# Optimization experiments

Hardware: AMD Instinct MI355X
Metric: run time of the kernel (lower is better)

## Reference

```python
import math
import jax, jax.numpy as jnp
import numpy as np

H = 8  # num_heads

def _layernorm(x, scale, bias, eps=1e-5):
    m = x.mean(-1, keepdims=True)
    v = x.var(-1, keepdims=True)
    return (x - m) / jnp.sqrt(v + eps) * scale + bias

def setup_inputs() -> dict:
    key = jax.random.key(0)
    ks = jax.random.split(key, 12)
    B, C, P, D, G = 8, 32, 256, 256, 512
    n = jax.random.normal
    return {
        "qz": n(ks[0], (B, C, P, D), dtype=jnp.float32),
        "unary": n(ks[1], (B, C, P, D), dtype=jnp.float32),
        # per-sample condition-instantiated factors; scaled ~1/sqrt(D) so attn logits are sane
        "time_u": n(ks[2], (B, D, D), dtype=jnp.float32) * 0.06,
        "time_v": n(ks[3], (B, D, D), dtype=jnp.float32) * 0.06,
        "channel_u": n(ks[4], (B, D, D), dtype=jnp.float32) * 0.06,
        "channel_v": n(ks[5], (B, D, D), dtype=jnp.float32) * 0.06,
        "topic_binary": n(ks[6], (B, G, D), dtype=jnp.float32) * 0.02,
        "norm_scale": jnp.ones((D,), jnp.float32),
        "norm_bias": jnp.zeros((D,), jnp.float32),
        "gate_w": n(ks[7], (D, D), dtype=jnp.float32) * 0.02,
        "gate_b": jnp.zeros((D,), jnp.float32),
        "out_w1": n(ks[8], (D, D), dtype=jnp.float32) * 0.02,
        "out_b1": jnp.zeros((D,), jnp.float32),
        "out_w2": n(ks[9], (D, D), dtype=jnp.float32) * 0.02,
        "out_b2": jnp.zeros((D,), jnp.float32),
    }

def reference(qz, unary, time_u, time_v, channel_u, channel_v, topic_binary,
              norm_scale, norm_bias, gate_w, gate_b, out_w1, out_b1, out_w2, out_b2):
    B, C, P, D = qz.shape
    R = D // H
    inv_sqrt_r = 1.0 / math.sqrt(R)

    qz_n = _layernorm(qz, norm_scale, norm_bias)

    def heads(x, w):  # [B,C,P,D] x [B,D,D] -> [B,C,P,H,R]
        return jnp.einsum('bcpd,bod->bcpo', x, w).reshape(B, C, P, H, R)

    # --- time-factor message: attention over P within each (b, c, h) ---
    qu = heads(qz_n, time_u).transpose(0, 1, 3, 2, 4)   # [B,C,H,P,R]
    qv = heads(qz_n, time_v).transpose(0, 1, 3, 2, 4)
    attn_t = jax.nn.softmax(jnp.einsum('bchpr,bchqr->bchpq', qu, qv) * inv_sqrt_r, axis=-1)
    m_t = jnp.einsum('bchpq,bcqd->bchpd', attn_t, qz_n).mean(axis=2)  # [B,C,P,D]

    # --- channel-factor message: attention over C within each (b, p, h) ---
    qu = heads(qz_n, channel_u).transpose(0, 2, 3, 1, 4)  # [B,P,H,C,R]
    qv = heads(qz_n, channel_v).transpose(0, 2, 3, 1, 4)
    attn_c = jax.nn.softmax(jnp.einsum('bphcr,bphfr->bphcf', qu, qv) * inv_sqrt_r, axis=-1)
    qzp = qz_n.transpose(0, 2, 1, 3)                      # [B,P,C,D]
    m_c = jnp.einsum('bphcf,bpfd->bphcd', attn_c, qzp).mean(axis=2).transpose(0, 2, 1, 3)

    # --- topic-modeling binary factor with AbsNormalize (relu + L1-normalize) ---
    qg = jax.nn.relu(jnp.einsum('bcpd,bgd->bcpg', qz_n, topic_binary))
    qg = qg / jnp.maximum(qg.sum(axis=-1, keepdims=True), 1e-6)
    m_g = jnp.einsum('bcpg,bgd->bcpd', qg, topic_binary)

    # --- gated residual update ---
    gate = jax.nn.sigmoid(qz @ gate_w.T + gate_b)
    qz2 = gate * qz + (1.0 - gate) * (unary + m_t + m_c + m_g)

    # --- output MLP with shared LayerNorm ---
    h = _layernorm(qz2, norm_scale, norm_bias)
    h = jax.nn.gelu(h @ out_w1.T + out_b1, approximate=False) @ out_w2.T + out_b2
    return qz2 + h
```

## Files before the change

kernel.cpp:

```cpp
#include <hip/hip_runtime.h>
#include <math.h>

namespace {

constexpr float INV_SQRT_R = 0.17677669529663689f;

typedef __attribute__((ext_vector_type(8))) __bf16 bf16x8;
typedef __attribute__((ext_vector_type(4))) float f32x4;

static __device__ __forceinline__ f32x4 MF(bf16x8 a, bf16x8 b, f32x4 c) {
    return __builtin_amdgcn_mfma_f32_16x16x32_bf16(a, b, c, 0, 0, 0);
}

__global__ __launch_bounds__(256) void cvt_kernel(
    const float* __restrict__ src, __bf16* __restrict__ dst, int n)
{
    int i = (blockIdx.x * 256 + threadIdx.x) * 4;
    if (i < n) {
        float4 v = *(const float4*)(src + i);
        dst[i + 0] = (__bf16)v.x; dst[i + 1] = (__bf16)v.y;
        dst[i + 2] = (__bf16)v.z; dst[i + 3] = (__bf16)v.w;
    }
}

__global__ __launch_bounds__(256) void cvt2_kernel(
    const float* __restrict__ src, __bf16* __restrict__ dst, int n,
    int dstChunk, int dstOff)
{
    int i = (blockIdx.x * 256 + threadIdx.x) * 4;
    if (i < n) {
        float4 v = *(const float4*)(src + i);
        int o = (i >> 16) * dstChunk + dstOff + (i & 65535);
        dst[o + 0] = (__bf16)v.x; dst[o + 1] = (__bf16)v.y;
        dst[o + 2] = (__bf16)v.z; dst[o + 3] = (__bf16)v.w;
    }
}

__global__ __launch_bounds__(256) void ln_kernel(
    const float* __restrict__ x, const float* __restrict__ sc,
    const float* __restrict__ bi, __bf16* __restrict__ y)
{
    const size_t row = blockIdx.x;
    const int t = threadIdx.x;
    const float v = x[row * 256 + t];
    float s = v, s2 = v * v;
    #pragma unroll
    for (int o = 32; o > 0; o >>= 1) {
        s  += __shfl_xor(s, o);
        s2 += __shfl_xor(s2, o);
    }
    __shared__ float ps[4], ps2[4];
    if ((t & 63) == 0) { ps[t >> 6] = s; ps2[t >> 6] = s2; }
    __syncthreads();
    const float S  = ps[0] + ps[1] + ps[2] + ps[3];
    const float S2 = ps2[0] + ps2[1] + ps2[2] + ps2[3];
    const float mean = S * (1.0f / 256.0f);
    const float var  = S2 * (1.0f / 256.0f) - mean * mean;
    const float inv  = 1.0f / sqrtf(var + 1e-5f);
    y[row * 256 + t] = (__bf16)((v - mean) * inv * sc[t] + bi[t]);
}

__global__ __launch_bounds__(256) void tpose_bf_kernel(
    const __bf16* __restrict__ src, __bf16* __restrict__ dst, int R, int C)
{
    const size_t bz = blockIdx.z;
    src += bz * (size_t)R * C;
    dst += bz * (size_t)R * C;
    __shared__ __bf16 tile[32][34];
    const int r0 = blockIdx.x * 32, c0 = blockIdx.y * 32;
    const int tx = threadIdx.x & 31, ty = threadIdx.x >> 5;
    #pragma unroll
    for (int i = 0; i < 32; i += 8)
        tile[ty + i][tx] = src[(size_t)(r0 + ty + i) * C + c0 + tx];
    __syncthreads();
    #pragma unroll
    for (int i = 0; i < 32; i += 8)
        dst[(size_t)(c0 + ty + i) * R + r0 + tx] = tile[tx][ty + i];
}

__global__ __launch_bounds__(256) void tpose_cvt_kernel(
    const float* __restrict__ src, __bf16* __restrict__ dst, int R, int C)
{
    const size_t bz = blockIdx.z;
    src += bz * (size_t)R * C;
    dst += bz * (size_t)R * C;
    __shared__ __bf16 tile[32][34];
    const int r0 = blockIdx.x * 32, c0 = blockIdx.y * 32;
    const int tx = threadIdx.x & 31, ty = threadIdx.x >> 5;
    #pragma unroll
    for (int i = 0; i < 32; i += 8)
        tile[ty + i][tx] = (__bf16)src[(size_t)(r0 + ty + i) * C + c0 + tx];
    __syncthreads();
    #pragma unroll
    for (int i = 0; i < 32; i += 8)
        dst[(size_t)(c0 + ty + i) * R + r0 + tx] = tile[tx][ty + i];
}

__global__ __launch_bounds__(256) void mgemm_kernel(
    const __bf16* __restrict__ A, const __bf16* __restrict__ Bm, __bf16* __restrict__ Cout,
    int K, size_t aStride, size_t bStride,
    size_t s_b, size_t s_c, size_t s_p, size_t s_w, size_t s_h)
{
    const int bb = blockIdx.z;
    const int m0 = blockIdx.x * 64;
    const int n0 = blockIdx.y * 256;
    const __bf16* Ab = A + (size_t)bb * aStride;
    const __bf16* Bb = Bm + (size_t)bb * bStride;
    __shared__ __align__(16) __bf16 As[64][40];
    __shared__ __align__(16) __bf16 Bs[256][40];
    const int t = threadIdx.x;
    const int lane = t & 63;
    const int wid = t >> 6;
    const int l15 = lane & 15, lg = lane >> 4;

    f32x4 acc[4][4] = {};

    for (int k0 = 0; k0 < K; k0 += 32) {
        {
            const int row = t >> 2, k8 = (t & 3) << 3;
            *(bf16x8*)&As[row][k8] = *(const bf16x8*)(Ab + (size_t)(m0 + row) * K + k0 + k8);
        }
        #pragma unroll
        for (int s = 0; s < 4; ++s) {
            const int slot = s * 256 + t;
            const int row = slot >> 2, k8 = (slot & 3) << 3;
            *(bf16x8*)&Bs[row][k8] = *(const bf16x8*)(Bb + (size_t)(n0 + row) * K + k0 + k8);
        }
        __syncthreads();
        bf16x8 af[4], bfr[4];
        #pragma unroll
        for (int i = 0; i < 4; ++i)
            af[i] = *(const bf16x8*)&As[i * 16 + l15][lg * 8];
        #pragma unroll
        for (int j = 0; j < 4; ++j)
            bfr[j] = *(const bf16x8*)&Bs[wid * 64 + j * 16 + l15][lg * 8];
        #pragma unroll
        for (int i = 0; i < 4; ++i)
            #pragma unroll
            for (int j = 0; j < 4; ++j)
                acc[i][j] = MF(af[i], bfr[j], acc[i][j]);
        __syncthreads();
    }

    #pragma unroll
    for (int j = 0; j < 4; ++j) {
        const int n = n0 + wid * 64 + j * 16 + l15;
        const size_t offn = (size_t)(n >> 8) * s_w + (size_t)((n >> 5) & 7) * s_h + (n & 31);
        #pragma unroll
        for (int i = 0; i < 4; ++i) {
            #pragma unroll
            for (int r = 0; r < 4; ++r) {
                const int m = m0 + i * 16 + lg * 4 + r;
                const size_t off = (size_t)bb * s_b + (size_t)(m >> 8) * s_c
                                 + (size_t)(m & 255) * s_p + offn;
                Cout[off] = (__bf16)acc[i][j][r];
            }
        }
    }
}

__global__ __launch_bounds__(256) void time_attn_mfma_kernel(
    const __bf16* __restrict__ qu, const __bf16* __restrict__ qv, __bf16* __restrict__ abar)
{
    const int bc = blockIdx.x;
    const int p0 = blockIdx.y * 64;
    const __bf16* quB = qu + (size_t)bc * 65536;
    const __bf16* qvB = qv + (size_t)bc * 65536;
    __shared__ __align__(16) __bf16 Us[64][40];
    __shared__ __align__(16) __bf16 Vs[256][40];
    const int t = threadIdx.x;
    const int lane = t & 63;
    const int wid = t >> 6;
    const int l15 = lane & 15, lg = lane >> 4;

    f32x4 acc[16] = {};

    for (int h = 0; h < 8; ++h) {
        const __bf16* quH = quB + h * 8192;
        const __bf16* qvH = qvB + h * 8192;
        __syncthreads();
        {
            const int row = t >> 2, k8 = (t & 3) << 3;
            *(bf16x8*)&Us[row][k8] = *(const bf16x8*)(quH + (size_t)(p0 + row) * 32 + k8);
        }
        #pragma unroll
        for (int i = 0; i < 4; ++i) {
            const int slot = i * 256 + t;
            const int row = slot >> 2, k8 = (slot & 3) << 3;
            *(bf16x8*)&Vs[row][k8] = *(const bf16x8*)(qvH + (size_t)row * 32 + k8);
        }
        __syncthreads();

        f32x4 s[16];
        bf16x8 a = *(const bf16x8*)&Us[wid * 16 + l15][lg * 8];
        #pragma unroll
        for (int j = 0; j < 16; ++j) {
            bf16x8 bfr = *(const bf16x8*)&Vs[j * 16 + l15][lg * 8];
            s[j] = MF(a, bfr, (f32x4){0.f, 0.f, 0.f, 0.f});
        }

        #pragma unroll
        for (int r = 0; r < 4; ++r) {
            float e[16];
            float sum = 0.0f;
            #pragma unroll
            for (int j = 0; j < 16; ++j) {
                e[j] = __expf(s[j][r] * INV_SQRT_R);
                sum += e[j];
            }
            sum += __shfl_xor(sum, 1);
            sum += __shfl_xor(sum, 2);
            sum += __shfl_xor(sum, 4);
            sum += __shfl_xor(sum, 8);
            const float inv = 0.125f / sum;
            #pragma unroll
            for (int j = 0; j < 16; ++j) acc[j][r] += e[j] * inv;
        }
    }

    __bf16* dst = abar + (size_t)bc * 65536 + (size_t)(p0 + wid * 16 + lg * 4) * 256 + l15;
    #pragma unroll
    for (int r = 0; r < 4; ++r)
        #pragma unroll
        for (int j = 0; j < 16; ++j)
            dst[(size_t)r * 256 + j * 16] = (__bf16)acc[j][r];
}

__global__ __launch_bounds__(256) void chan_fused_kernel(
    const __bf16* __restrict__ quc, const __bf16* __restrict__ qvc,
    const __bf16* __restrict__ qzn, __bf16* __restrict__ m_c)
{
    const int bp = blockIdx.x;
    const int b = bp >> 8, p = bp & 255;
    const __bf16* quB = quc + (size_t)bp * 8192;
    const __bf16* qvB = qvc + (size_t)bp * 8192;
    __shared__ float U[16896];
    __shared__ float ab[32 * 33];
    float* qus = U;
    float* qvs = U + 8448;
    const int t = threadIdx.x;
    #pragma unroll
    for (int i = 0; i < 4; ++i) {
        int fi = i * 256 + t;
        int e = fi << 3;
        bf16x8 a = *(const bf16x8*)(quB + e);
        bf16x8 bv = *(const bf16x8*)(qvB + e);
        int base = ((e >> 10) * 32 + ((e >> 5) & 31)) * 33 + (e & 31);
        #pragma unroll
        for (int j = 0; j < 8; ++j) {
            qus[base + j] = (float)a[j];
            qvs[base + j] = (float)bv[j];
        }
    }
    __syncthreads();
    const int c = t >> 3, j = t & 7;
    float acc[4] = {0.f, 0.f, 0.f, 0.f};
    for (int h = 0; h < 8; ++h) {
        float qur[32];
        #pragma unroll
        for (int r = 0; r < 32; ++r) qur[r] = qus[(h * 32 + c) * 33 + r];
        float s[4];
        #pragma unroll
        for (int jj = 0; jj < 4; ++jj) {
            int f = j * 4 + jj;
            const float* qvR = &qvs[(h * 32 + f) * 33];
            float a = 0.f;
            #pragma unroll
            for (int r = 0; r < 32; ++r) a += qur[r] * qvR[r];
            s[jj] = a * INV_SQRT_R;
        }
        float mx = fmaxf(fmaxf(s[0], s[1]), fmaxf(s[2], s[3]));
        mx = fmaxf(mx, __shfl_xor(mx, 1));
        mx = fmaxf(mx, __shfl_xor(mx, 2));
        mx = fmaxf(mx, __shfl_xor(mx, 4));
        float e0x = __expf(s[0] - mx), e1x = __expf(s[1] - mx);
        float e2x = __expf(s[2] - mx), e3x = __expf(s[3] - mx);
        float sum = e0x + e1x + e2x + e3x;
        sum += __shfl_xor(sum, 1);
        sum += __shfl_xor(sum, 2);
        sum += __shfl_xor(sum, 4);
        float inv = 0.125f / sum;
        acc[0] += e0x * inv; acc[1] += e1x * inv; acc[2] += e2x * inv; acc[3] += e3x * inv;
    }
    #pragma unroll
    for (int jj = 0; jj < 4; ++jj) ab[c * 33 + j * 4 + jj] = acc[jj];
    __syncthreads();
    float* bt = U;
    #pragma unroll 4
    for (int f = 0; f < 32; ++f)
        bt[f * 256 + t] = (float)qzn[((size_t)(b * 32 + f) * 256 + p) * 256 + t];
    __syncthreads();
    for (int c2 = 0; c2 < 32; c2 += 2) {
        float a0 = 0.f, a1 = 0.f;
        #pragma unroll
        for (int f = 0; f < 32; ++f) {
            float v = bt[f * 256 + t];
            a0 += ab[c2 * 33 + f] * v;
            a1 += ab[(c2 + 1) * 33 + f] * v;
        }
        size_t off = ((size_t)(b * 32 + c2) * 256 + p) * 256 + t;
        m_c[off] = (__bf16)a0;
        m_c[off + 65536] = (__bf16)a1;
    }
}

__global__ __launch_bounds__(256, 2) void topic_fused_kernel(
    const __bf16* __restrict__ qzn, const __bf16* __restrict__ topicb,
    const __bf16* __restrict__ topicTb, __bf16* __restrict__ m_g)
{
    const int bb = blockIdx.z;
    const int m0 = blockIdx.x * 32;
    const __bf16* Ab = qzn + (size_t)bb * 2097152;
    const __bf16* B1 = topicb + (size_t)bb * 131072;
    const __bf16* B2 = topicTb + (size_t)bb * 131072;
    __shared__ __align__(16) __bf16 As[32][40];
    __shared__ __align__(16) __bf16 Bs[512][40];
    __shared__ __align__(16) __bf16 Ps[32][520];
    __shared__ float rsInv[32];
    const int t = threadIdx.x;
    const int lane = t & 63, wid = t >> 6;
    const int l15 = lane & 15, lg = lane >> 4;

    f32x4 acc[2][8] = {};
    for (int k0 = 0; k0 < 256; k0 += 32) {
        if (t < 128) {
            const int row = t >> 2, k8 = (t & 3) << 3;
            *(bf16x8*)&As[row][k8] = *(const bf16x8*)(Ab + (size_t)(m0 + row) * 256 + k0 + k8);
        }
        #pragma unroll
        for (int s = 0; s < 8; ++s) {
            const int slot = s * 256 + t;
            const int row = slot >> 2, k8 = (slot & 3) << 3;
            *(bf16x8*)&Bs[row][k8] = *(const bf16x8*)(B1 + (size_t)row * 256 + k0 + k8);
        }
        __syncthreads();
        bf16x8 af0 = *(const bf16x8*)&As[l15][lg * 8];
        bf16x8 af1 = *(const bf16x8*)&As[16 + l15][lg * 8];
        #pragma unroll
        for (int j = 0; j < 8; ++j) {
            bf16x8 b8 = *(const bf16x8*)&Bs[wid * 128 + j * 16 + l15][lg * 8];
            acc[0][j] = MF(af0, b8, acc[0][j]);
            acc[1][j] = MF(af1, b8, acc[1][j]);
        }
        __syncthreads();
    }
    #pragma unroll
    for (int i = 0; i < 2; ++i)
        #pragma unroll
        for (int j = 0; j < 8; ++j) {
            const int n = wid * 128 + j * 16 + l15;
            #pragma unroll
            for (int r = 0; r < 4; ++r)
                Ps[i * 16 + lg * 4 + r][n] = (__bf16)fmaxf(acc[i][j][r], 0.0f);
        }
    __syncthreads();
    {
        const int row = t >> 3, seg = t & 7;
        float s = 0.0f;
        #pragma unroll
        for (int u = 0; u < 8; ++u) {
            bf16x8 v = *(const bf16x8*)&Ps[row][seg * 64 + u * 8];
            #pragma unroll
            for (int e = 0; e < 8; ++e) s += (float)v[e];
        }
        s += __shfl_xor(s, 1);
        s += __shfl_xor(s, 2);
        s += __shfl_xor(s, 4);
        if (seg == 0) rsInv[row] = 1.0f / fmaxf(s, 1e-6f);
    }
    __syncthreads();
    f32x4 acc2[2][4] = {};
    for (int k0 = 0; k0 < 512; k0 += 32) {
        #pragma unroll
        for (int s = 0; s < 4; ++s) {
            const int slot = s * 256 + t;
            const int row = slot >> 2, k8 = (slot & 3) << 3;
            *(bf16x8*)&Bs[row][k8] = *(const bf16x8*)(B2 + (size_t)row * 512 + k0 + k8);
        }
        __syncthreads();
        bf16x8 af0 = *(const bf16x8*)&Ps[l15][k0 + lg * 8];
        bf16x8 af1 = *(const bf16x8*)&Ps[16 + l15][k0 + lg * 8];
        #pragma unroll
        for (int j = 0; j < 4; ++j) {
            bf16x8 b8 = *(const bf16x8*)&Bs[wid * 64 + j * 16 + l15][lg * 8];
            acc2[0][j] = MF(af0, b8, acc2[0][j]);
            acc2[1][j] = MF(af1, b8, acc2[1][j]);
        }
        __syncthreads();
    }
    #pragma unroll
    for (int i = 0; i < 2; ++i)
        #pragma unroll
        for (int j = 0; j < 4; ++j) {
            const int n = wid * 64 + j * 16 + l15;
            #pragma unroll
            for (int r = 0; r < 4; ++r) {
                const int ml = i * 16 + lg * 4 + r;
                m_g[(size_t)bb * 2097152 + (size_t)(m0 + ml) * 256 + n]
                    = (__bf16)(acc2[i][j][r] * rsInv[ml]);
            }
        }
}

__global__ __launch_bounds__(256, 2) void mega_kernel(
    const __bf16* __restrict__ qzb, const float* __restrict__ unary,
    const __bf16* __restrict__ m_t, const __bf16* __restrict__ m_c,
    const __bf16* __restrict__ m_g,
    const __bf16* __restrict__ gwb, const float* __restrict__ gate_b,
    const __bf16* __restrict__ w1b, const float* __restrict__ b1,
    const __bf16* __restrict__ w2b, const float* __restrict__ b2,
    const float* __restrict__ nsc, const float* __restrict__ nbi,
    float* __restrict__ outp)
{
    const int m0 = blockIdx.x * 64;
    __shared__ __align__(16) __bf16 As[64][40];
    __shared__ __align__(16) __bf16 Bs[256][40];
    __shared__ __align__(16) __bf16 hL[64][264];
    __shared__ float lnp[64][4][2];
    const int t = threadIdx.x;
    const int lane = t & 63, wid = t >> 6;
    const int l15 = lane & 15, lg = lane >> 4;

    f32x4 acc[4][4] = {};
    for (int k0 = 0; k0 < 256; k0 += 32) {
        {
            const int row = t >> 2, k8 = (t & 3) << 3;
            *(bf16x8*)&As[row][k8] = *(const bf16x8*)(qzb + (size_t)(m0 + row) * 256 + k0 + k8);
        }
        #pragma unroll
        for (int s = 0; s < 4; ++s) {
            const int slot = s * 256 + t;
            const int row = slot >> 2, k8 = (slot & 3) << 3;
            *(bf16x8*)&Bs[row][k8] = *(const bf16x8*)(gwb + (size_t)row * 256 + k0 + k8);
        }
        __syncthreads();
        bf16x8 af[4], bfr[4];
        #pragma unroll
        for (int i = 0; i < 4; ++i) af[i] = *(const bf16x8*)&As[i * 16 + l15][lg * 8];
        #pragma unroll
        for (int j = 0; j < 4; ++j) bfr[j] = *(const bf16x8*)&Bs[wid * 64 + j * 16 + l15][lg * 8];
        #pragma unroll
        for (int i = 0; i < 4; ++i)
            #pragma unroll
            for (int j = 0; j < 4; ++j)
                acc[i][j] = MF(af[i], bfr[j], acc[i][j]);
        __syncthreads();
    }

    f32x4 z2[4][4];
    #pragma unroll
    for (int i = 0; i < 4; ++i) {
        #pragma unroll
        for (int r = 0; r < 4; ++r) {
            float s = 0.0f, s2 = 0.0f;
            #pragma unroll
            for (int j = 0; j < 4; ++j) {
                const int n = wid * 64 + j * 16 + l15;
                const size_t off = (size_t)(m0 + i * 16 + lg * 4 + r) * 256 + n;
                float g = 1.0f / (1.0f + __expf(-(acc[i][j][r] + gate_b[n])));
                float rest = unary[off] + (float)m_t[off] + (float)m_c[off] + (float)m_g[off];
                float v = g * (float)qzb[off] + (1.0f - g) * rest;
                z2[i][j][r] = v;
                s += v; s2 += v * v;
            }
            s  += __shfl_xor(s, 1);  s  += __shfl_xor(s, 2);
            s  += __shfl_xor(s, 4);  s  += __shfl_xor(s, 8);
            s2 += __shfl_xor(s2, 1); s2 += __shfl_xor(s2, 2);
            s2 += __shfl_xor(s2, 4); s2 += __shfl_xor(s2, 8);
            if (l15 == 0) {
                lnp[i * 16 + lg * 4 + r][wid][0] = s;
                lnp[i * 16 + lg * 4 + r][wid][1] = s2;
            }
        }
    }
    __syncthreads();
    #pragma unroll
    for (int i = 0; i < 4; ++i) {
        #pragma unroll
        for (int r = 0; r < 4; ++r) {
            const int rr = i * 16 + lg * 4 + r;
            float S  = lnp[rr][0][0] + lnp[rr][1][0] + lnp[rr][2][0] + lnp[rr][3][0];
            float S2 = lnp[rr][0][1] + lnp[rr][1][1] + lnp[rr][2][1] + lnp[rr][3][1];
            float mean = S * (1.0f / 256.0f);
            float var  = S2 * (1.0f / 256.0f) - mean * mean;
            float inv  = 1.0f / sqrtf(var + 1e-5f);
            #pragma unroll
            for (int j = 0; j < 4; ++j) {
                const int n = wid * 64 + j * 16 + l15;
                hL[rr][n] = (__bf16)((z2[i][j][r] - mean) * inv * nsc[n] + nbi[n]);
            }
        }
    }
    __syncthreads();

    f32x4 acc2[4][4] = {};
    for (int k0 = 0; k0 < 256; k0 += 32) {
        #pragma unroll
        for (int s = 0; s < 4; ++s) {
            const int slot = s * 256 + t;
            const int row = slot >> 2, k8 = (slot & 3) << 3;
            *(bf16x8*)&Bs[row][k8] = *(const bf16x8*)(w1b + (size_t)row * 256 + k0 + k8);
        }
        __syncthreads();
        bf16x8 af[4], bfr[4];
        #pragma unroll
        for (int i = 0; i < 4; ++i) af[i] = *(const bf16x8*)&hL[i * 16 + l15][k0 + lg * 8];
        #pragma unroll
        for (int j = 0; j < 4; ++j) bfr[j] = *(const bf16x8*)&Bs[wid * 64 + j * 16 + l15][lg * 8];
        #pragma unroll
        for (int i = 0; i < 4; ++i)
            #pragma unroll
            for (int j = 0; j < 4; ++j)
                acc2[i][j] = MF(af[i], bfr[j], acc2[i][j]);
        __syncthreads();
    }
    #pragma unroll
    for (int i = 0; i < 4; ++i)
        #pragma unroll
        for (int j = 0; j < 4; ++j) {
            const int n = wid * 64 + j * 16 + l15;
            const float bn = b1[n];
            #pragma unroll
            for (int r = 0; r < 4; ++r) {
                float x = acc2[i][j][r] + bn;
                hL[i * 16 + lg * 4 + r][n] = (__bf16)(0.5f * x * (1.0f + erff(x * 0.7071067811865475f)));
            }
        }
    __syncthreads();

    f32x4 acc3[4][4] = {};
    for (int k0 = 0; k0 < 256; k0 += 32) {
        #pragma unroll
        for (int s = 0; s < 4; ++s) {
            const int slot = s * 256 + t;
            const int row = slot >> 2, k8 = (slot & 3) << 3;
            *(bf16x8*)&Bs[row][k8] = *(const bf16x8*)(w2b + (size_t)row * 256 + k0 + k8);
        }
        __syncthreads();
        bf16x8 af[4], bfr[4];
        #pragma unroll
        for (int i = 0; i < 4; ++i) af[i] = *(const bf16x8*)&hL[i * 16 + l15][k0 + lg * 8];
        #pragma unroll
        for (int j = 0; j < 4; ++j) bfr[j] = *(const bf16x8*)&Bs[wid * 64 + j * 16 + l15][lg * 8];
        #pragma unroll
        for (int i = 0; i < 4; ++i)
            #pragma unroll
            for (int j = 0; j < 4; ++j)
                acc3[i][j] = MF(af[i], bfr[j], acc3[i][j]);
        __syncthreads();
    }
    #pragma unroll
    for (int i = 0; i < 4; ++i)
        #pragma unroll
        for (int j = 0; j < 4; ++j) {
            const int n = wid * 64 + j * 16 + l15;
            const float bn = b2[n];
            #pragma unroll
            for (int r = 0; r < 4; ++r) {
                const size_t off = (size_t)(m0 + i * 16 + lg * 4 + r) * 256 + n;
                outp[off] = z2[i][j][r] + acc3[i][j][r] + bn;
            }
        }
}

}

extern "C" void kernel_launch(void* const* d_in, const int* in_sizes, int n_in,
                              void* d_out, int out_size, void* d_ws, size_t ws_size,
                              hipStream_t stream)
{
    (void)in_sizes; (void)n_in; (void)out_size; (void)ws_size;
    const float* qz     = (const float*)d_in[0];
    const float* unary  = (const float*)d_in[1];
    const float* time_u = (const float*)d_in[2];
    const float* time_v = (const float*)d_in[3];
    const float* chan_u = (const float*)d_in[4];
    const float* chan_v = (const float*)d_in[5];
    const float* topic  = (const float*)d_in[6];
    const float* nsc    = (const float*)d_in[7];
    const float* nbi    = (const float*)d_in[8];
    const float* gate_w = (const float*)d_in[9];
    const float* gate_b = (const float*)d_in[10];
    const float* w1     = (const float*)d_in[11];
    const float* b1     = (const float*)d_in[12];
    const float* w2     = (const float*)d_in[13];
    const float* b2     = (const float*)d_in[14];

    char* base = (char*)d_ws;
    __bf16* qzn_b  = (__bf16*)base;
    __bf16* pool   = (__bf16*)(base + (32ull << 20));
    __bf16* wtime  = pool;
    __bf16* wchan  = pool + 1048576;
    __bf16* topicb = pool + 2097152;
    __bf16* topicTb= pool + 3145728;
    __bf16* gwb    = pool + 4194304;
    __bf16* w1b    = pool + 4259840;
    __bf16* w2b    = pool + 4325376;
    __bf16* Blo    = (__bf16*)(base + (64ull << 20));
    __bf16* Bhi    = (__bf16*)(base + (96ull << 20));
    __bf16* qu_t   = Blo;
    __bf16* qv_t   = Bhi;
    __bf16* qznT   = Blo;
    __bf16* qu_c   = Blo;
    __bf16* qv_c   = Bhi;
    __bf16* qzb    = Blo;
    __bf16* m_g    = Bhi;
    __bf16* m_t    = (__bf16*)(base + (128ull << 20));
    __bf16* m_c    = (__bf16*)(base + (160ull << 20));
    __bf16* abar   = (__bf16*)d_out;
    float*  OUTF   = (float*)d_out;

    dim3 blk(256);

    cvt2_kernel<<<512, blk, 0, stream>>>(time_u, wtime, 524288, 131072, 0);
    cvt2_kernel<<<512, blk, 0, stream>>>(time_v, wtime, 524288, 131072, 65536);
    cvt2_kernel<<<512, blk, 0, stream>>>(chan_u, wchan, 524288, 131072, 0);
    cvt2_kernel<<<512, blk, 0, stream>>>(chan_v, wchan, 524288, 131072, 65536);
    cvt_kernel<<<1024, blk, 0, stream>>>(topic, topicb, 1048576);
    tpose_cvt_kernel<<<dim3(16, 8, 8), blk, 0, stream>>>(topic, topicTb, 512, 256);
    cvt_kernel<<<64, blk, 0, stream>>>(gate_w, gwb, 65536);
    cvt_kernel<<<64, blk, 0, stream>>>(w1, w1b, 65536);
    cvt_kernel<<<64, blk, 0, stream>>>(w2, w2b, 65536);

    ln_kernel<<<65536, blk, 0, stream>>>(qz, nsc, nbi, qzn_b);

    mgemm_kernel<<<dim3(128, 2, 8), blk, 0, stream>>>(
        qzn_b, wtime, qu_t, 256, 2097152, 131072,
        2097152, 65536, 32, 16777216, 8192);

    time_attn_mfma_kernel<<<dim3(256, 4), blk, 0, stream>>>(qu_t, qv_t, abar);

    tpose_bf_kernel<<<dim3(8, 8, 256), blk, 0, stream>>>(qzn_b, qznT, 256, 256);

    mgemm_kernel<<<dim3(4, 1, 256), blk, 0, stream>>>(
        abar, qznT, m_t, 256, 65536, 65536,
        65536, 0, 256, 0, 32);

    mgemm_kernel<<<dim3(128, 2, 8), blk, 0, stream>>>(
        qzn_b, wchan, qu_c, 256, 2097152, 131072,
        2097152, 32, 8192, 16777216, 1024);

    chan_fused_kernel<<<2048, blk, 0, stream>>>(qu_c, qv_c, qzn_b, m_c);

    topic_fused_kernel<<<dim3(256, 1, 8), blk, 0, stream>>>(qzn_b, topicb, topicTb, m_g);

    cvt_kernel<<<16384, blk, 0, stream>>>(qz, qzb, 16777216);

    mega_kernel<<<1024, blk, 0, stream>>>(
        qzb, unary, m_t, m_c, m_g,
        gwb, gate_b, w1b, b1, w2b, b2, nsc, nbi, OUTF);
}
```

Measured before the change: 589.3 us.

## Fuse time-attention with m_t GEMM and fold qz conversion into mega kernel

The time-attention kernel now keeps its head-averaged attention matrix in shared memory and multiplies it directly by the transposed normalized input, removing the intermediate abar write/read and a separate GEMM launch. The mega kernel reads fp32 qz and converts it to bf16 in shared memory, eliminating a standalone conversion pass. The channel kernel stores q tiles as bf16 with vector loads instead of scalar fp32 expansion. Workspace buffers are re-aliased to fit the new schedule, and the larger shared memory footprint may reduce occupancy.

```diff
diff --git a/kernel.cpp b/kernel.cpp
--- a/kernel.cpp
+++ b/kernel.cpp
@@ -159,15 +159,20 @@
     }
 }
 
-__global__ __launch_bounds__(256) void time_attn_mfma_kernel(
-    const __bf16* __restrict__ qu, const __bf16* __restrict__ qv, __bf16* __restrict__ abar)
+__global__ __launch_bounds__(256) void time_attn_mt_kernel(
+    const __bf16* __restrict__ qu, const __bf16* __restrict__ qv,
+    const __bf16* __restrict__ qznT, __bf16* __restrict__ m_t)
 {
     const int bc = blockIdx.x;
     const int p0 = blockIdx.y * 64;
     const __bf16* quB = qu + (size_t)bc * 65536;
     const __bf16* qvB = qv + (size_t)bc * 65536;
-    __shared__ __align__(16) __bf16 Us[64][40];
-    __shared__ __align__(16) __bf16 Vs[256][40];
+    const __bf16* BT  = qznT + (size_t)bc * 65536;
+    __shared__ __align__(16) __bf16 R1[27136];
+    __bf16* Us  = R1;
+    __bf16* Vs  = R1 + 2560;
+    __bf16* aL  = R1;
+    __bf16* Bs2 = R1 + 16896;
     const int t = threadIdx.x;
     const int lane = t & 63;
     const int wid = t >> 6;
@@ -181,21 +186,21 @@
         __syncthreads();
         {
             const int row = t >> 2, k8 = (t & 3) << 3;
-            *(bf16x8*)&Us[row][k8] = *(const bf16x8*)(quH + (size_t)(p0 + row) * 32 + k8);
+            *(bf16x8*)&Us[row * 40 + k8] = *(const bf16x8*)(quH + (size_t)(p0 + row) * 32 + k8);
         }
         #pragma unroll
         for (int i = 0; i < 4; ++i) {
             const int slot = i * 256 + t;
             const int row = slot >> 2, k8 = (slot & 3) << 3;
-            *(bf16x8*)&Vs[row][k8] = *(const bf16x8*)(qvH + (size_t)row * 32 + k8);
+            *(bf16x8*)&Vs[row * 40 + k8] = *(const bf16x8*)(qvH + (size_t)row * 32 + k8);
         }
         __syncthreads();
 
         f32x4 s[16];
-        bf16x8 a = *(const bf16x8*)&Us[wid * 16 + l15][lg * 8];
+        bf16x8 a = *(const bf16x8*)&Us[(wid * 16 + l15) * 40 + lg * 8];
         #pragma unroll
         for (int j = 0; j < 16; ++j) {
-            bf16x8 bfr = *(const bf16x8*)&Vs[j * 16 + l15][lg * 8];
+            bf16x8 bfr = *(const bf16x8*)&Vs[(j * 16 + l15) * 40 + lg * 8];
             s[j] = MF(a, bfr, (f32x4){0.f, 0.f, 0.f, 0.f});
         }
 
@@ -218,12 +223,50 @@
         }
     }
 
-    __bf16* dst = abar + (size_t)bc * 65536 + (size_t)(p0 + wid * 16 + lg * 4) * 256 + l15;
-    #pragma unroll
-    for (int r = 0; r < 4; ++r)
+    __syncthreads();
+    #pragma unroll
+    for (int r = 0; r < 4; ++r) {
+        const int row = wid * 16 + lg * 4 + r;
         #pragma unroll
         for (int j = 0; j < 16; ++j)
-            dst[(size_t)r * 256 + j * 16] = (__bf16)acc[j][r];
+            aL[row * 264 + j * 16 + l15] = (__bf16)acc[j][r];
+    }
+    __syncthreads();
+
+    f32x4 acc2[4][4] = {};
+    for (int k0 = 0; k0 < 256; k0 += 32) {
+        #pragma unroll
+        for (int s = 0; s < 4; ++s) {
+            const int slot = s * 256 + t;
+            const int row = slot >> 2, k8 = (slot & 3) << 3;
+            *(bf16x8*)&Bs2[row * 40 + k8] = *(const bf16x8*)(BT + (size_t)row * 256 + k0 + k8);
+        }
+        __syncthreads();
+        bf16x8 af[4], bfr[4];
+        #pragma unroll
+        for (int i = 0; i < 4; ++i)
+            af[i] = *(const bf16x8*)&aL[(i * 16 + l15) * 264 + k0 + lg * 8];
+        #pragma unroll
+        for (int j = 0; j < 4; ++j)
+            bfr[j] = *(const bf16x8*)&Bs2[(wid * 64 + j * 16 + l15) * 40 + lg * 8];
+        #pragma unroll
+        for (int i = 0; i < 4; ++i)
+            #pragma unroll
+            for (int j = 0; j < 4; ++j)
+                acc2[i][j] = MF(af[i], bfr[j], acc2[i][j]);
+        __syncthreads();
+    }
+    #pragma unroll
+    for (int i = 0; i < 4; ++i)
+        #pragma unroll
+        for (int j = 0; j < 4; ++j) {
+            const int d = wid * 64 + j * 16 + l15;
+            #pragma unroll
+            for (int r = 0; r < 4; ++r) {
+                const int p = p0 + i * 16 + lg * 4 + r;
+                m_t[(size_t)bc * 65536 + (size_t)p * 256 + d] = (__bf16)acc2[i][j][r];
+            }
+        }
 }
 
 __global__ __launch_bounds__(256) void chan_fused_kernel(
@@ -234,23 +277,19 @@
     const int b = bp >> 8, p = bp & 255;
     const __bf16* quB = quc + (size_t)bp * 8192;
     const __bf16* qvB = qvc + (size_t)bp * 8192;
-    __shared__ float U[16896];
+    __shared__ __align__(16) __bf16 QU[20480];
     __shared__ float ab[32 * 33];
-    float* qus = U;
-    float* qvs = U + 8448;
+    __bf16* qus = QU;
+    __bf16* qvs = QU + 10240;
     const int t = threadIdx.x;
     #pragma unroll
     for (int i = 0; i < 4; ++i) {
         int fi = i * 256 + t;
         int e = fi << 3;
-        bf16x8 a = *(const bf16x8*)(quB + e);
-        bf16x8 bv = *(const bf16x8*)(qvB + e);
-        int base = ((e >> 10) * 32 + ((e >> 5) & 31)) * 33 + (e & 31);
-        #pragma unroll
-        for (int j = 0; j < 8; ++j) {
-            qus[base + j] = (float)a[j];
-            qvs[base + j] = (float)bv[j];
-        }
+        int h = e >> 10, cc = (e >> 5) & 31, r = e & 31;
+        int base = (h * 32 + cc) * 40 + r;
+        *(bf16x8*)&qus[base] = *(const bf16x8*)(quB + e);
+        *(bf16x8*)&qvs[base] = *(const bf16x8*)(qvB + e);
     }
     __syncthreads();
     const int c = t >> 3, j = t & 7;
@@ -258,15 +297,22 @@
     for (int h = 0; h < 8; ++h) {
         float qur[32];
         #pragma unroll
-        for (int r = 0; r < 32; ++r) qur[r] = qus[(h * 32 + c) * 33 + r];
+        for (int u = 0; u < 4; ++u) {
+            bf16x8 q8 = *(const bf16x8*)&qus[(h * 32 + c) * 40 + u * 8];
+            #pragma unroll
+            for (int e2 = 0; e2 < 8; ++e2) qur[u * 8 + e2] = (float)q8[e2];
+        }
         float s[4];
         #pragma unroll
         for (int jj = 0; jj < 4; ++jj) {
             int f = j * 4 + jj;
-            const float* qvR = &qvs[(h * 32 + f) * 33];
             float a = 0.f;
             #pragma unroll
-            for (int r = 0; r < 32; ++r) a += qur[r] * qvR[r];
+            for (int u = 0; u < 4; ++u) {
+                bf16x8 v8 = *(const bf16x8*)&qvs[(h * 32 + f) * 40 + u * 8];
+                #pragma unroll
+                for (int e2 = 0; e2 < 8; ++e2) a += qur[u * 8 + e2] * (float)v8[e2];
+            }
             s[jj] = a * INV_SQRT_R;
         }
         float mx = fmaxf(fmaxf(s[0], s[1]), fmaxf(s[2], s[3]));
@@ -285,7 +331,7 @@
     #pragma unroll
     for (int jj = 0; jj < 4; ++jj) ab[c * 33 + j * 4 + jj] = acc[jj];
     __syncthreads();
-    float* bt = U;
+    float* bt = (float*)QU;
     #pragma unroll 4
     for (int f = 0; f < 32; ++f)
         bt[f * 256 + t] = (float)qzn[((size_t)(b * 32 + f) * 256 + p) * 256 + t];
@@ -403,7 +449,7 @@
 }
 
 __global__ __launch_bounds__(256, 2) void mega_kernel(
-    const __bf16* __restrict__ qzb, const float* __restrict__ unary,
+    const float* __restrict__ qz, const float* __restrict__ unary,
     const __bf16* __restrict__ m_t, const __bf16* __restrict__ m_c,
     const __bf16* __restrict__ m_g,
     const __bf16* __restrict__ gwb, const float* __restrict__ gate_b,
@@ -413,7 +459,6 @@
     float* __restrict__ outp)
 {
     const int m0 = blockIdx.x * 64;
-    __shared__ __align__(16) __bf16 As[64][40];
     __shared__ __align__(16) __bf16 Bs[256][40];
     __shared__ __align__(16) __bf16 hL[64][264];
     __shared__ float lnp[64][4][2];
@@ -421,12 +466,22 @@
     const int lane = t & 63, wid = t >> 6;
     const int l15 = lane & 15, lg = lane >> 4;
 
+    #pragma unroll
+    for (int s = 0; s < 8; ++s) {
+        const int slot = s * 256 + t;
+        const int row = slot >> 5;
+        const int k8 = (slot & 31) << 3;
+        const float* src = qz + (size_t)(m0 + row) * 256 + k8;
+        float4 v0 = *(const float4*)src;
+        float4 v1 = *(const float4*)(src + 4);
+        bf16x8 pk;
+        pk[0] = (__bf16)v0.x; pk[1] = (__bf16)v0.y; pk[2] = (__bf16)v0.z; pk[3] = (__bf16)v0.w;
+        pk[4] = (__bf16)v1.x; pk[5] = (__bf16)v1.y; pk[6] = (__bf16)v1.z; pk[7] = (__bf16)v1.w;
+        *(bf16x8*)&hL[row][k8] = pk;
+    }
+
     f32x4 acc[4][4] = {};
     for (int k0 = 0; k0 < 256; k0 += 32) {
-        {
-            const int row = t >> 2, k8 = (t & 3) << 3;
-            *(bf16x8*)&As[row][k8] = *(const bf16x8*)(qzb + (size_t)(m0 + row) * 256 + k0 + k8);
-        }
         #pragma unroll
         for (int s = 0; s < 4; ++s) {
             const int slot = s * 256 + t;
@@ -436,7 +491,7 @@
         __syncthreads();
         bf16x8 af[4], bfr[4];
         #pragma unroll
-        for (int i = 0; i < 4; ++i) af[i] = *(const bf16x8*)&As[i * 16 + l15][lg * 8];
+        for (int i = 0; i < 4; ++i) af[i] = *(const bf16x8*)&hL[i * 16 + l15][k0 + lg * 8];
         #pragma unroll
         for (int j = 0; j < 4; ++j) bfr[j] = *(const bf16x8*)&Bs[wid * 64 + j * 16 + l15][lg * 8];
         #pragma unroll
@@ -452,14 +507,15 @@
     for (int i = 0; i < 4; ++i) {
         #pragma unroll
         for (int r = 0; r < 4; ++r) {
+            const int rr = i * 16 + lg * 4 + r;
             float s = 0.0f, s2 = 0.0f;
             #pragma unroll
             for (int j = 0; j < 4; ++j) {
                 const int n = wid * 64 + j * 16 + l15;
-                const size_t off = (size_t)(m0 + i * 16 + lg * 4 + r) * 256 + n;
+                const size_t off = (size_t)(m0 + rr) * 256 + n;
                 float g = 1.0f / (1.0f + __expf(-(acc[i][j][r] + gate_b[n])));
                 float rest = unary[off] + (float)m_t[off] + (float)m_c[off] + (float)m_g[off];
-                float v = g * (float)qzb[off] + (1.0f - g) * rest;
+                float v = g * (float)hL[rr][n] + (1.0f - g) * rest;
                 z2[i][j][r] = v;
                 s += v; s2 += v * v;
             }
@@ -468,8 +524,8 @@
             s2 += __shfl_xor(s2, 1); s2 += __shfl_xor(s2, 2);
             s2 += __shfl_xor(s2, 4); s2 += __shfl_xor(s2, 8);
             if (l15 == 0) {
-                lnp[i * 16 + lg * 4 + r][wid][0] = s;
-                lnp[i * 16 + lg * 4 + r][wid][1] = s2;
+                lnp[rr][wid][0] = s;
+                lnp[rr][wid][1] = s2;
             }
         }
     }
@@ -600,14 +656,12 @@
     __bf16* Bhi    = (__bf16*)(base + (96ull << 20));
     __bf16* qu_t   = Blo;
     __bf16* qv_t   = Bhi;
-    __bf16* qznT   = Blo;
     __bf16* qu_c   = Blo;
     __bf16* qv_c   = Bhi;
-    __bf16* qzb    = Blo;
-    __bf16* m_g    = Bhi;
-    __bf16* m_t    = (__bf16*)(base + (128ull << 20));
-    __bf16* m_c    = (__bf16*)(base + (160ull << 20));
-    __bf16* abar   = (__bf16*)d_out;
+    __bf16* m_g    = Blo;
+    __bf16* qznT   = (__bf16*)(base + (128ull << 20));
+    __bf16* m_c    = qznT;
+    __bf16* m_t    = (__bf16*)(base + (160ull << 20));
     float*  OUTF   = (float*)d_out;
 
     dim3 blk(256);
@@ -623,18 +677,13 @@
     cvt_kernel<<<64, blk, 0, stream>>>(w2, w2b, 65536);
 
     ln_kernel<<<65536, blk, 0, stream>>>(qz, nsc, nbi, qzn_b);
+    tpose_bf_kernel<<<dim3(8, 8, 256), blk, 0, stream>>>(qzn_b, qznT, 256, 256);
 
     mgemm_kernel<<<dim3(128, 2, 8), blk, 0, stream>>>(
         qzn_b, wtime, qu_t, 256, 2097152, 131072,
         2097152, 65536, 32, 16777216, 8192);
 
-    time_attn_mfma_kernel<<<dim3(256, 4), blk, 0, stream>>>(qu_t, qv_t, abar);
-
-    tpose_bf_kernel<<<dim3(8, 8, 256), blk, 0, stream>>>(qzn_b, qznT, 256, 256);
-
-    mgemm_kernel<<<dim3(4, 1, 256), blk, 0, stream>>>(
-        abar, qznT, m_t, 256, 65536, 65536,
-        65536, 0, 256, 0, 32);
+    time_attn_mt_kernel<<<dim3(256, 4), blk, 0, stream>>>(qu_t, qv_t, qznT, m_t);
 
     mgemm_kernel<<<dim3(128, 2, 8), blk, 0, stream>>>(
         qzn_b, wchan, qu_c, 256, 2097152, 131072,
@@ -644,9 +693,7 @@
 
     topic_fused_kernel<<<dim3(256, 1, 8), blk, 0, stream>>>(qzn_b, topicb, topicTb, m_g);
 
-    cvt_kernel<<<16384, blk, 0, stream>>>(qz, qzb, 16777216);
-
     mega_kernel<<<1024, blk, 0, stream>>>(
-        qzb, unary, m_t, m_c, m_g,
+        qz, unary, m_t, m_c, m_g,
         gwb, gate_b, w1b, b1, w2b, b2, nsc, nbi, OUTF);
 }
```

After: 540.7 us. 8.3% less time.
